# Optimization experiments

Measured on AMD Instinct MI355X. Metric: run time of the kernel, lower is better.

The kernel has to match this reference:

```python
import jax, jax.numpy as jnp
import numpy as np

B, D, H = 1024, 512, 128
S = D - 1
PI = float(np.pi)


def setup_inputs() -> dict:
    key = jax.random.key(0)
    k = jax.random.split(key, 4)
    # angles on the circle [0, 2*pi)
    z = jax.random.uniform(k[0], (B, D), dtype=jnp.float32) * (2.0 * PI)
    W1 = jax.random.normal(k[1], (S, D, H), dtype=jnp.float32) * 0.05
    b1 = jnp.zeros((S, H), dtype=jnp.float32)
    W2 = jax.random.normal(k[2], (S, H, 2), dtype=jnp.float32) * 0.05
    b2 = jnp.zeros((S, 2), dtype=jnp.float32)
    return {"z": z, "W1": W1, "b1": b1, "W2": W2, "b2": b2}


def reference(z, W1, b1, W2, b2):
    """IterativeARLayer.decode: sequential per-site conditioner + NCP diffeomorphism.

    Step idx conditions on z[:, :idx] (implemented as an input mask, identical math)
    and transforms site idx, accumulating log|det|.
    """
    Bn, Dn = z.shape
    Sn = Dn - 1
    # conditioner mask for step s transforms site idx=s+1, conditions on sites 0..s
    mask = (jnp.arange(Dn)[None, :] <= jnp.arange(Sn)[:, None]).astype(z.dtype)  # [S, D]
    idxs = jnp.arange(1, Dn)

    def step(carry, xs):
        x, log_det = carry
        w1, bb1, w2, bb2, m, idx = xs
        h = jax.nn.relu((z * m) @ w1 + bb1)          # [B, H]
        p = h @ w2 + bb2                              # [B, 2] unconstrained params
        alpha_raw, beta = p[:, 0], p[:, 1]
        a = jnp.exp(alpha_raw)
        # NCP diffeomorphism on site idx
        phi = z[:, idx]                               # [B]
        u = jnp.tan(0.5 * (phi - PI))
        v = a * u + beta
        out = 2.0 * jnp.arctan(v) + PI
        ld = alpha_raw + jnp.log1p(u * u) - jnp.log1p(v * v)
        x = x.at[:, idx].set(out)
        return (x, log_det + ld), None

    init = (z, jnp.zeros((Bn,), dtype=z.dtype))  # x = z.clone(); site 0 untouched
    (x, log_det), _ = jax.lax.scan(step, init, (W1, b1, W2, b2, mask, idxs))
    return x, log_det
```

## Files before the change

### kernel.cpp

```cpp
#include <hip/hip_runtime.h>
#include <math.h>

#define B_DIM 1024
#define D_DIM 512
#define H_DIM 128
#define S_DIM 511
#define PI_F 3.14159265358979323846f
#define ZSWZ_BYTES (8u * 1024u * 128u)
#define NTILES_TOTAL 2296
#define W1BF_BYTES ((size_t)NTILES_TOTAL * 16384)

typedef __attribute__((ext_vector_type(8))) short short8;
typedef __attribute__((ext_vector_type(4))) float f32x4;

static __device__ __forceinline__ unsigned cvt_pk_bf16(float lo, float hi) {
    unsigned r;
    asm("v_cvt_pk_bf16_f32 %0, %1, %2" : "=v"(r) : "v"(lo), "v"(hi));
    return r;
}

static __device__ __host__ __forceinline__ int tiles_before(int s) {
    const int q = s >> 6, r = s & 63;
    return s + 32 * q * (q - 1) + q * r;
}

__global__ __launch_bounds__(256) void pack_kernel(
        const float* __restrict__ z, const float* __restrict__ W1,
        unsigned char* __restrict__ z_swz, unsigned char* __restrict__ w1bf)
{
    if (blockIdx.x < 256) {
        const int gid = blockIdx.x * 256 + threadIdx.x;
        const int g   = gid & 7;
        const int row = (gid >> 3) & 1023;
        const int kt  = gid >> 13;
        const int srcg = g ^ (row & 7);
        const float* src = z + (size_t)row * D_DIM + kt * 64 + srcg * 8;
        float4 a = *(const float4*)src;
        float4 b = *(const float4*)(src + 4);
        uint4 w;
        w.x = cvt_pk_bf16(a.x, a.y);
        w.y = cvt_pk_bf16(a.z, a.w);
        w.z = cvt_pk_bf16(b.x, b.y);
        w.w = cvt_pk_bf16(b.z, b.w);
        *(uint4*)(z_swz + (size_t)kt * 131072 + row * 128 + g * 16) = w;
        return;
    }
    const int tb = blockIdx.x - 256;
    const int s  = tb >> 3;
    const int kk = tb & 7;
    if (s >= S_DIM || kk > (s >> 6)) return;
    const int k0 = kk << 6;
    const int t  = threadIdx.x;
    const int h2 = t & 63;
    const int mw = t >> 6;
    const float* __restrict__ W1s = W1 + (size_t)s * (D_DIM * H_DIM);
    unsigned char* out = w1bf + (size_t)(tiles_before(s) + kk) * 16384;
    const int h0 = h2 * 2, h1 = h2 * 2 + 1;
#pragma unroll
    for (int half = 0; half < 2; ++half) {
        const int m = mw + half * 4;
        float2 v[8];
#pragma unroll
        for (int e = 0; e < 8; ++e) {
            const int gk = k0 + m * 8 + e;
            v[e] = (gk <= s) ? *(const float2*)(W1s + (size_t)gk * H_DIM + h0)
                             : (float2){0.f, 0.f};
        }
        uint4 w0, w1;
        w0.x = cvt_pk_bf16(v[0].x, v[1].x); w0.y = cvt_pk_bf16(v[2].x, v[3].x);
        w0.z = cvt_pk_bf16(v[4].x, v[5].x); w0.w = cvt_pk_bf16(v[6].x, v[7].x);
        w1.x = cvt_pk_bf16(v[0].y, v[1].y); w1.y = cvt_pk_bf16(v[2].y, v[3].y);
        w1.z = cvt_pk_bf16(v[4].y, v[5].y); w1.w = cvt_pk_bf16(v[6].y, v[7].y);
        *(uint4*)(out + h0 * 128 + ((m ^ (h0 & 7)) << 4)) = w0;
        *(uint4*)(out + h1 * 128 + ((m ^ (h1 & 7)) << 4)) = w1;
    }
}

template<bool PRE>
__global__ __launch_bounds__(256) void ar_site_kernel(
        const float* __restrict__ z, const unsigned char* __restrict__ z_swz,
        const unsigned char* __restrict__ w1bf,
        const float* __restrict__ W1, const float* __restrict__ b1,
        const float* __restrict__ W2, const float* __restrict__ b2,
        float* __restrict__ x_out, float* __restrict__ ld_out)
{
    __shared__ __align__(16) unsigned char lds[73728];

    const int tid  = threadIdx.x;
    const int lane = tid & 63;
    const int wid  = tid >> 6;
    const int wr   = wid >> 1;
    const int wc   = wid & 1;
    const int l15  = lane & 15;
    const int l16  = lane >> 4;

    if (PRE) {
        const int ib   = blockIdx.x;
        const int c    = (((ib >> 3) & 7) << 3) | (ib & 7);
        const int bblk = ib >> 6;
        const int brow0 = bblk * 128;

        int pf_t = 0, pf_kk = 0, pf_step = 0;
        int pf_s = 510 - c;
        int pf_base = tiles_before(pf_s);

        auto pf_stage = [&]() {
            if (pf_t >= 8) return;
            const int slot = pf_step & 1;
            const unsigned char* srcA = z_swz + (size_t)pf_kk * 131072
                                        + (size_t)brow0 * 128 + wid * 4096 + lane * 16;
            const unsigned char* srcB = w1bf + (size_t)(pf_base + pf_kk) * 16384
                                        + wid * 4096 + lane * 16;
            unsigned char* dstA = lds + slot * 32768 + wid * 4096;
            unsigned char* dstB = lds + slot * 32768 + 16384 + wid * 4096;
#pragma unroll
            for (int i2 = 0; i2 < 4; ++i2) {
                __builtin_amdgcn_global_load_lds(
                    (const __attribute__((address_space(1))) unsigned int*)(srcA + i2 * 1024),
                    (__attribute__((address_space(3))) unsigned int*)(dstA + i2 * 1024),
                    16, 0, 0);
                __builtin_amdgcn_global_load_lds(
                    (const __attribute__((address_space(1))) unsigned int*)(srcB + i2 * 1024),
                    (__attribute__((address_space(3))) unsigned int*)(dstB + i2 * 1024),
                    16, 0, 0);
            }
            ++pf_step; ++pf_kk;
            if (pf_kk == ((pf_s >> 6) + 1)) {
                pf_kk = 0; ++pf_t;
                while (pf_t < 8) {
                    const int j = pf_t * 64 + ((pf_t & 1) ? (63 - c) : c);
                    if (j < S_DIM) { pf_s = 510 - j; pf_base = tiles_before(pf_s); break; }
                    ++pf_t;
                }
            }
        };

        int csteps = 0;
#pragma unroll
        for (int t = 0; t < 8; ++t) {
            const int j = t * 64 + ((t & 1) ? (63 - c) : c);
            if (j < S_DIM) csteps += ((510 - j) >> 6) + 1;
        }

        pf_stage();
        pf_stage();

        int step = 0;
        float ld_acc = 0.f;

        for (int t = 0; t < 8; ++t) {
            const int j = t * 64 + ((t & 1) ? (63 - c) : c);
            if (j >= S_DIM) continue;
            const int s   = 510 - j;
            const int nt  = (s >> 6) + 1;
            const int idx = s + 1;

            f32x4 acc[4][4];
#pragma unroll
            for (int mi = 0; mi < 4; ++mi)
#pragma unroll
                for (int ni = 0; ni < 4; ++ni)
                    acc[mi][ni] = (f32x4){0.f, 0.f, 0.f, 0.f};

            for (int kk = 0; kk < nt; ++kk) {
                if (step + 1 == csteps) {
                    asm volatile("s_waitcnt vmcnt(0)" ::: "memory");
                } else {
                    asm volatile("s_waitcnt vmcnt(8)" ::: "memory");
                }
                __builtin_amdgcn_s_barrier();
                __builtin_amdgcn_sched_barrier(0);
                const unsigned char* bufp = lds + (step & 1) * 32768;
#pragma unroll
                for (int ks = 0; ks < 2; ++ks) {
                    const int kb = ks * 64 + l16 * 16;
                    short8 af[4], bfr[4];
#pragma unroll
                    for (int mi = 0; mi < 4; ++mi) {
                        const int r = wr * 64 + mi * 16 + l15;
                        af[mi] = *(const short8*)(bufp + r * 128 + (kb ^ ((r & 7) << 4)));
                    }
#pragma unroll
                    for (int ni = 0; ni < 4; ++ni) {
                        const int h = wc * 64 + ni * 16 + l15;
                        bfr[ni] = *(const short8*)(bufp + 16384 + h * 128 + (kb ^ ((h & 7) << 4)));
                    }
                    __builtin_amdgcn_s_setprio(1);
#pragma unroll
                    for (int mi = 0; mi < 4; ++mi)
#pragma unroll
                        for (int ni = 0; ni < 4; ++ni)
                            acc[mi][ni] = __builtin_amdgcn_mfma_f32_16x16x32_bf16(
                                af[mi], bfr[ni], acc[mi][ni], 0, 0, 0);
                    __builtin_amdgcn_s_setprio(0);
                }
                __builtin_amdgcn_s_barrier();
                pf_stage();
                ++step;
            }

            float b1v[4], w2a[4], w2b[4];
#pragma unroll
            for (int ni = 0; ni < 4; ++ni) {
                const int cc = wc * 64 + ni * 16 + l15;
                b1v[ni] = b1[(size_t)s * H_DIM + cc];
                const float2 w2v = *(const float2*)(W2 + ((size_t)s * H_DIM + cc) * 2);
                w2a[ni] = w2v.x;
                w2b[ni] = w2v.y;
            }
            float p0s[4][4], p1s[4][4];
#pragma unroll
            for (int mi = 0; mi < 4; ++mi)
#pragma unroll
                for (int r = 0; r < 4; ++r) {
                    float p0 = 0.f, p1 = 0.f;
#pragma unroll
                    for (int ni = 0; ni < 4; ++ni) {
                        float h = acc[mi][ni][r] + b1v[ni];
                        h = fmaxf(h, 0.f);
                        p0 = fmaf(h, w2a[ni], p0);
                        p1 = fmaf(h, w2b[ni], p1);
                    }
                    p0s[mi][r] = p0; p1s[mi][r] = p1;
                }
#pragma unroll
            for (int mi = 0; mi < 4; ++mi)
#pragma unroll
                for (int r = 0; r < 4; ++r) {
                    p0s[mi][r] += __shfl_xor(p0s[mi][r], 1);
                    p0s[mi][r] += __shfl_xor(p0s[mi][r], 2);
                    p1s[mi][r] += __shfl_xor(p1s[mi][r], 1);
                    p1s[mi][r] += __shfl_xor(p1s[mi][r], 2);
                }
            if ((lane & 3) == 0) {
                const int cw = wc * 4 + (l15 >> 2);
#pragma unroll
                for (int mi = 0; mi < 4; ++mi)
#pragma unroll
                    for (int r = 0; r < 4; ++r) {
                        const int row = wr * 64 + mi * 16 + l16 * 4 + r;
                        *(float2*)(lds + 65536 + (row * 8 + (cw ^ (row & 7))) * 8)
                            = (float2){p0s[mi][r], p1s[mi][r]};
                    }
            }
            asm volatile("s_waitcnt lgkmcnt(0)" ::: "memory");
            __builtin_amdgcn_s_barrier();
            __builtin_amdgcn_sched_barrier(0);
            if (tid < 128) {
                const int row = tid;
                float alpha = b2[(size_t)s * 2 + 0];
                float beta  = b2[(size_t)s * 2 + 1];
#pragma unroll
                for (int cw = 0; cw < 8; ++cw) {
                    const float2 v = *(const float2*)(lds + 65536 + (row * 8 + (cw ^ (row & 7))) * 8);
                    alpha += v.x; beta += v.y;
                }
                const int grow = brow0 + row;
                const float phi = z[(size_t)grow * D_DIM + idx];
                const float u = tanf(0.5f * (phi - PI_F));
                const float a = expf(alpha);
                const float v = fmaf(a, u, beta);
                x_out[(size_t)grow * D_DIM + idx] = 2.0f * atanf(v) + PI_F;
                ld_acc += alpha + log1pf(u * u) - log1pf(v * v);
            }
        }
        if (tid < 128) atomicAdd(ld_out + brow0 + tid, ld_acc);
        if (c == 0 && tid < 128)
            x_out[(size_t)(brow0 + tid) * D_DIM] = z[(size_t)(brow0 + tid) * D_DIM];
        return;
    }

    const int ib    = blockIdx.x;
    const int s_idx = ((ib >> 6) << 3) | (ib & 7);
    if (s_idx >= S_DIM) return;
    const int s     = S_DIM - 1 - s_idx;
    const int bblk  = (ib >> 3) & 7;
    const int brow0 = bblk * 128;
    const int K     = s + 1;
    const int idx   = s + 1;
    const float* __restrict__ W1s = W1 + (size_t)s * (D_DIM * H_DIM);

    f32x4 acc[4][4];
#pragma unroll
    for (int mi = 0; mi < 4; ++mi)
#pragma unroll
        for (int ni = 0; ni < 4; ++ni)
            acc[mi][ni] = (f32x4){0.f, 0.f, 0.f, 0.f};

    const int ntiles = (K + 63) >> 6;
    for (int kk = 0; kk < ntiles; ++kk) {
        const int k0 = kk << 6;
        const int g  = tid & 7;
        const int rb = tid >> 3;
#pragma unroll
        for (int p = 0; p < 4; ++p) {
            const int row  = p * 32 + rb;
            const int srcg = g ^ (row & 7);
            const float* zp = z + (size_t)(brow0 + row) * D_DIM + k0 + srcg * 8;
            float4 va = *(const float4*)zp;
            float4 vb = *(const float4*)(zp + 4);
            uint4 w;
            w.x = cvt_pk_bf16(va.x, va.y);
            w.y = cvt_pk_bf16(va.z, va.w);
            w.z = cvt_pk_bf16(vb.x, vb.y);
            w.w = cvt_pk_bf16(vb.z, vb.w);
            *(uint4*)(lds + row * 128 + g * 16) = w;
        }
        const int hgrp  = tid & 31;
        const int kgrp  = tid >> 5;
        const int kbase = k0 + kgrp * 8;
        const float* wp = W1s + (size_t)kbase * H_DIM + hgrp * 4;
        float4 cc[8];
#pragma unroll
        for (int jj = 0; jj < 8; ++jj) {
            float4 v = *(const float4*)(wp + (size_t)jj * H_DIM);
            const bool ok = (kbase + jj) < K;
            v.x = ok ? v.x : 0.f;  v.y = ok ? v.y : 0.f;
            v.z = ok ? v.z : 0.f;  v.w = ok ? v.w : 0.f;
            cc[jj] = v;
        }
        const float* cf = (const float*)cc;
#pragma unroll
        for (int i2 = 0; i2 < 4; ++i2) {
            const int h = hgrp * 4 + i2;
            uint4 w;
            w.x = cvt_pk_bf16(cf[0 * 4 + i2], cf[1 * 4 + i2]);
            w.y = cvt_pk_bf16(cf[2 * 4 + i2], cf[3 * 4 + i2]);
            w.z = cvt_pk_bf16(cf[4 * 4 + i2], cf[5 * 4 + i2]);
            w.w = cvt_pk_bf16(cf[6 * 4 + i2], cf[7 * 4 + i2]);
            *(uint4*)(lds + 16384 + h * 128 + ((kgrp * 16) ^ ((h & 7) << 4))) = w;
        }
        __syncthreads();
#pragma unroll
        for (int ks = 0; ks < 2; ++ks) {
            const int kb = ks * 64 + l16 * 16;
            short8 af[4], bfr[4];
#pragma unroll
            for (int mi = 0; mi < 4; ++mi) {
                const int r = wr * 64 + mi * 16 + l15;
                af[mi] = *(const short8*)(lds + r * 128 + (kb ^ ((r & 7) << 4)));
            }
#pragma unroll
            for (int ni = 0; ni < 4; ++ni) {
                const int h = wc * 64 + ni * 16 + l15;
                bfr[ni] = *(const short8*)(lds + 16384 + h * 128 + (kb ^ ((h & 7) << 4)));
            }
#pragma unroll
            for (int mi = 0; mi < 4; ++mi)
#pragma unroll
                for (int ni = 0; ni < 4; ++ni)
                    acc[mi][ni] = __builtin_amdgcn_mfma_f32_16x16x32_bf16(
                        af[mi], bfr[ni], acc[mi][ni], 0, 0, 0);
        }
        __syncthreads();
    }

    float b1v[4], w2a[4], w2b[4];
#pragma unroll
    for (int ni = 0; ni < 4; ++ni) {
        const int cc2 = wc * 64 + ni * 16 + l15;
        b1v[ni] = b1[(size_t)s * H_DIM + cc2];
        const float* w2p = W2 + ((size_t)s * H_DIM + cc2) * 2;
        w2a[ni] = w2p[0];
        w2b[ni] = w2p[1];
    }
    float p0s[4][4], p1s[4][4];
#pragma unroll
    for (int mi = 0; mi < 4; ++mi)
#pragma unroll
        for (int r = 0; r < 4; ++r) {
            float p0 = 0.f, p1 = 0.f;
#pragma unroll
            for (int ni = 0; ni < 4; ++ni) {
                float h = acc[mi][ni][r] + b1v[ni];
                h = fmaxf(h, 0.f);
                p0 = fmaf(h, w2a[ni], p0);
                p1 = fmaf(h, w2b[ni], p1);
            }
            p0s[mi][r] = p0; p1s[mi][r] = p1;
        }
#pragma unroll
    for (int mi = 0; mi < 4; ++mi)
#pragma unroll
        for (int r = 0; r < 4; ++r) {
            p0s[mi][r] += __shfl_xor(p0s[mi][r], 1);
            p0s[mi][r] += __shfl_xor(p0s[mi][r], 2);
            p1s[mi][r] += __shfl_xor(p1s[mi][r], 1);
            p1s[mi][r] += __shfl_xor(p1s[mi][r], 2);
        }
    if ((lane & 3) == 0) {
        const int cw = wc * 4 + (l15 >> 2);
#pragma unroll
        for (int mi = 0; mi < 4; ++mi)
#pragma unroll
            for (int r = 0; r < 4; ++r) {
                const int row = wr * 64 + mi * 16 + l16 * 4 + r;
                *(float2*)(lds + 65536 + (row * 8 + (cw ^ (row & 7))) * 8)
                    = (float2){p0s[mi][r], p1s[mi][r]};
            }
    }
    __syncthreads();
    if (tid < 128) {
        const int row = tid;
        float alpha = b2[(size_t)s * 2 + 0];
        float beta  = b2[(size_t)s * 2 + 1];
#pragma unroll
        for (int cw = 0; cw < 8; ++cw) {
            const float2 v = *(const float2*)(lds + 65536 + (row * 8 + (cw ^ (row & 7))) * 8);
            alpha += v.x; beta += v.y;
        }
        const int grow = brow0 + row;
        const float phi = z[(size_t)grow * D_DIM + idx];
        const float u = tanf(0.5f * (phi - PI_F));
        const float a = expf(alpha);
        const float v = fmaf(a, u, beta);
        x_out[(size_t)grow * D_DIM + idx] = 2.0f * atanf(v) + PI_F;
        atomicAdd(ld_out + grow, alpha + log1pf(u * u) - log1pf(v * v));
        if (s_idx == 0)
            x_out[(size_t)grow * D_DIM] = z[(size_t)grow * D_DIM];
    }
}

extern "C" void kernel_launch(void* const* d_in, const int* in_sizes, int n_in,
                              void* d_out, int out_size, void* d_ws, size_t ws_size,
                              hipStream_t stream) {
    const float* z  = (const float*)d_in[0];
    const float* W1 = (const float*)d_in[1];
    const float* b1 = (const float*)d_in[2];
    const float* W2 = (const float*)d_in[3];
    const float* b2 = (const float*)d_in[4];
    float* x_out  = (float*)d_out;
    float* ld_out = x_out + (size_t)B_DIM * D_DIM;

    unsigned char* z_swz = (unsigned char*)d_ws;
    unsigned char* w1bf  = z_swz + ZSWZ_BYTES;
    const size_t need = ZSWZ_BYTES + W1BF_BYTES;

    hipMemsetAsync(ld_out, 0, B_DIM * sizeof(float), stream);
    if (ws_size >= need) {
        pack_kernel<<<dim3(256 + 4088), dim3(256), 0, stream>>>(z, W1, z_swz, w1bf);
        ar_site_kernel<true><<<dim3(512), dim3(256), 0, stream>>>(
            z, z_swz, w1bf, W1, b1, W2, b2, x_out, ld_out);
    } else {
        ar_site_kernel<false><<<dim3(4096), dim3(256), 0, stream>>>(
            z, nullptr, nullptr, W1, b1, W2, b2, x_out, ld_out);
    }
}
```

Before: 107.3 us.

## Use 32-wide K tiles, 8-wave blocks and 4-stage LDS prefetch pipeline

Repacks z and W1 into 32-wide K tiles with a new swizzle and tile indexing, and moves the precomputed path to 512-thread blocks. Each wave now computes a 64x32 slice, and the prefetch is split so half the waves load A and half load B. The double buffer becomes a 4-slot ring with three tiles in flight, one barrier per K step and graded vmcnt waits. The aim is to hide global-load latency and raise wave-level parallelism per CU. The cost is more K iterations, finer-grained loads, a wider shuffle reduction in the epilogue and more register pressure per block.

```diff
diff --git a/kernel.cpp b/kernel.cpp
--- a/kernel.cpp
+++ b/kernel.cpp
@@ -6,12 +6,18 @@
 #define H_DIM 128
 #define S_DIM 511
 #define PI_F 3.14159265358979323846f
-#define ZSWZ_BYTES (8u * 1024u * 128u)
-#define NTILES_TOTAL 2296
-#define W1BF_BYTES ((size_t)NTILES_TOTAL * 16384)
+#define ZSWZ_BYTES (16u * 1024u * 64u)
+#define NT32_TOTAL 4336
+#define W1BF_BYTES ((size_t)NT32_TOTAL * 8192)
+#define EPI_OFF 65536
 
 typedef __attribute__((ext_vector_type(8))) short short8;
 typedef __attribute__((ext_vector_type(4))) float f32x4;
+
+#define GLDS16(src, dst)                                                        \
+    __builtin_amdgcn_global_load_lds(                                           \
+        (const __attribute__((address_space(1))) unsigned int*)(src),           \
+        (__attribute__((address_space(3))) unsigned int*)(dst), 16, 0, 0)
 
 static __device__ __forceinline__ unsigned cvt_pk_bf16(float lo, float hi) {
     unsigned r;
@@ -19,9 +25,9 @@
     return r;
 }
 
-static __device__ __host__ __forceinline__ int tiles_before(int s) {
-    const int q = s >> 6, r = s & 63;
-    return s + 32 * q * (q - 1) + q * r;
+static __device__ __forceinline__ int tb32(int s) {
+    const int q = s >> 5, r = s & 31;
+    return 16 * q * (q + 1) + r * (q + 1);
 }
 
 __global__ __launch_bounds__(256) void pack_kernel(
@@ -30,11 +36,11 @@
 {
     if (blockIdx.x < 256) {
         const int gid = blockIdx.x * 256 + threadIdx.x;
-        const int g   = gid & 7;
-        const int row = (gid >> 3) & 1023;
-        const int kt  = gid >> 13;
-        const int srcg = g ^ (row & 7);
-        const float* src = z + (size_t)row * D_DIM + kt * 64 + srcg * 8;
+        const int g   = gid & 3;
+        const int row = (gid >> 2) & 1023;
+        const int kt  = gid >> 12;
+        const int srcg = g ^ ((row >> 1) & 3);
+        const float* src = z + (size_t)row * D_DIM + kt * 32 + srcg * 8;
         float4 a = *(const float4*)src;
         float4 b = *(const float4*)(src + 4);
         uint4 w;
@@ -42,42 +48,39 @@
         w.y = cvt_pk_bf16(a.z, a.w);
         w.z = cvt_pk_bf16(b.x, b.y);
         w.w = cvt_pk_bf16(b.z, b.w);
-        *(uint4*)(z_swz + (size_t)kt * 131072 + row * 128 + g * 16) = w;
+        *(uint4*)(z_swz + (size_t)kt * 65536 + row * 64 + g * 16) = w;
         return;
     }
     const int tb = blockIdx.x - 256;
-    const int s  = tb >> 3;
-    const int kk = tb & 7;
-    if (s >= S_DIM || kk > (s >> 6)) return;
-    const int k0 = kk << 6;
+    const int s  = tb >> 4;
+    const int kk = tb & 15;
+    if (s >= S_DIM || kk > (s >> 5)) return;
+    const int k0 = kk << 5;
     const int t  = threadIdx.x;
     const int h2 = t & 63;
     const int mw = t >> 6;
     const float* __restrict__ W1s = W1 + (size_t)s * (D_DIM * H_DIM);
-    unsigned char* out = w1bf + (size_t)(tiles_before(s) + kk) * 16384;
+    unsigned char* out = w1bf + (size_t)(tb32(s) + kk) * 8192;
     const int h0 = h2 * 2, h1 = h2 * 2 + 1;
-#pragma unroll
-    for (int half = 0; half < 2; ++half) {
-        const int m = mw + half * 4;
-        float2 v[8];
-#pragma unroll
-        for (int e = 0; e < 8; ++e) {
-            const int gk = k0 + m * 8 + e;
-            v[e] = (gk <= s) ? *(const float2*)(W1s + (size_t)gk * H_DIM + h0)
-                             : (float2){0.f, 0.f};
-        }
-        uint4 w0, w1;
-        w0.x = cvt_pk_bf16(v[0].x, v[1].x); w0.y = cvt_pk_bf16(v[2].x, v[3].x);
-        w0.z = cvt_pk_bf16(v[4].x, v[5].x); w0.w = cvt_pk_bf16(v[6].x, v[7].x);
-        w1.x = cvt_pk_bf16(v[0].y, v[1].y); w1.y = cvt_pk_bf16(v[2].y, v[3].y);
-        w1.z = cvt_pk_bf16(v[4].y, v[5].y); w1.w = cvt_pk_bf16(v[6].y, v[7].y);
-        *(uint4*)(out + h0 * 128 + ((m ^ (h0 & 7)) << 4)) = w0;
-        *(uint4*)(out + h1 * 128 + ((m ^ (h1 & 7)) << 4)) = w1;
-    }
+    const int slot = mw ^ (h2 & 3);
+    float2 v[8];
+#pragma unroll
+    for (int e = 0; e < 8; ++e) {
+        const int gk = k0 + mw * 8 + e;
+        v[e] = (gk <= s) ? *(const float2*)(W1s + (size_t)gk * H_DIM + h0)
+                         : (float2){0.f, 0.f};
+    }
+    uint4 w0, w1;
+    w0.x = cvt_pk_bf16(v[0].x, v[1].x); w0.y = cvt_pk_bf16(v[2].x, v[3].x);
+    w0.z = cvt_pk_bf16(v[4].x, v[5].x); w0.w = cvt_pk_bf16(v[6].x, v[7].x);
+    w1.x = cvt_pk_bf16(v[0].y, v[1].y); w1.y = cvt_pk_bf16(v[2].y, v[3].y);
+    w1.z = cvt_pk_bf16(v[4].y, v[5].y); w1.w = cvt_pk_bf16(v[6].y, v[7].y);
+    *(uint4*)(out + h0 * 64 + slot * 16) = w0;
+    *(uint4*)(out + h1 * 64 + slot * 16) = w1;
 }
 
 template<bool PRE>
-__global__ __launch_bounds__(256) void ar_site_kernel(
+__global__ __launch_bounds__(512, 4) void ar_site_kernel(
         const float* __restrict__ z, const unsigned char* __restrict__ z_swz,
         const unsigned char* __restrict__ w1bf,
         const float* __restrict__ W1, const float* __restrict__ b1,
@@ -89,12 +92,12 @@
     const int tid  = threadIdx.x;
     const int lane = tid & 63;
     const int wid  = tid >> 6;
-    const int wr   = wid >> 1;
-    const int wc   = wid & 1;
     const int l15  = lane & 15;
     const int l16  = lane >> 4;
 
     if (PRE) {
+        const int wr   = wid >> 2;
+        const int wc   = wid & 3;
         const int ib   = blockIdx.x;
         const int c    = (((ib >> 3) & 7) << 3) | (ib & 7);
         const int bblk = ib >> 6;
@@ -102,34 +105,31 @@
 
         int pf_t = 0, pf_kk = 0, pf_step = 0;
         int pf_s = 510 - c;
-        int pf_base = tiles_before(pf_s);
+        int pf_base = tb32(pf_s);
 
         auto pf_stage = [&]() {
             if (pf_t >= 8) return;
-            const int slot = pf_step & 1;
-            const unsigned char* srcA = z_swz + (size_t)pf_kk * 131072
-                                        + (size_t)brow0 * 128 + wid * 4096 + lane * 16;
-            const unsigned char* srcB = w1bf + (size_t)(pf_base + pf_kk) * 16384
-                                        + wid * 4096 + lane * 16;
-            unsigned char* dstA = lds + slot * 32768 + wid * 4096;
-            unsigned char* dstB = lds + slot * 32768 + 16384 + wid * 4096;
-#pragma unroll
-            for (int i2 = 0; i2 < 4; ++i2) {
-                __builtin_amdgcn_global_load_lds(
-                    (const __attribute__((address_space(1))) unsigned int*)(srcA + i2 * 1024),
-                    (__attribute__((address_space(3))) unsigned int*)(dstA + i2 * 1024),
-                    16, 0, 0);
-                __builtin_amdgcn_global_load_lds(
-                    (const __attribute__((address_space(1))) unsigned int*)(srcB + i2 * 1024),
-                    (__attribute__((address_space(3))) unsigned int*)(dstB + i2 * 1024),
-                    16, 0, 0);
+            unsigned char* slotp = lds + (pf_step & 3) * 16384;
+            if (wid < 4) {
+                const unsigned char* srcA = z_swz + (size_t)pf_kk * 65536
+                    + (size_t)(brow0 + wid * 32) * 64 + lane * 16;
+                unsigned char* dstA = slotp + wid * 2048;
+                GLDS16(srcA, dstA);
+                GLDS16(srcA + 1024, dstA + 1024);
+            } else {
+                const int w2 = wid - 4;
+                const unsigned char* srcB = w1bf + (size_t)(pf_base + pf_kk) * 8192
+                    + (size_t)(w2 * 32) * 64 + lane * 16;
+                unsigned char* dstB = slotp + 8192 + w2 * 2048;
+                GLDS16(srcB, dstB);
+                GLDS16(srcB + 1024, dstB + 1024);
             }
             ++pf_step; ++pf_kk;
-            if (pf_kk == ((pf_s >> 6) + 1)) {
+            if (pf_kk == (pf_s >> 5) + 1) {
                 pf_kk = 0; ++pf_t;
                 while (pf_t < 8) {
                     const int j = pf_t * 64 + ((pf_t & 1) ? (63 - c) : c);
-                    if (j < S_DIM) { pf_s = 510 - j; pf_base = tiles_before(pf_s); break; }
+                    if (j < S_DIM) { pf_s = 510 - j; pf_base = tb32(pf_s); break; }
                     ++pf_t;
                 }
             }
@@ -139,11 +139,10 @@
 #pragma unroll
         for (int t = 0; t < 8; ++t) {
             const int j = t * 64 + ((t & 1) ? (63 - c) : c);
-            if (j < S_DIM) csteps += ((510 - j) >> 6) + 1;
-        }
-
-        pf_stage();
-        pf_stage();
+            if (j < S_DIM) csteps += ((510 - j) >> 5) + 1;
+        }
+
+        pf_stage(); pf_stage(); pf_stage();
 
         int step = 0;
         float ld_acc = 0.f;
@@ -152,96 +151,83 @@
             const int j = t * 64 + ((t & 1) ? (63 - c) : c);
             if (j >= S_DIM) continue;
             const int s   = 510 - j;
-            const int nt  = (s >> 6) + 1;
+            const int nt  = (s >> 5) + 1;
             const int idx = s + 1;
 
-            f32x4 acc[4][4];
+            f32x4 acc[4][2];
 #pragma unroll
             for (int mi = 0; mi < 4; ++mi)
 #pragma unroll
-                for (int ni = 0; ni < 4; ++ni)
+                for (int ni = 0; ni < 2; ++ni)
                     acc[mi][ni] = (f32x4){0.f, 0.f, 0.f, 0.f};
 
             for (int kk = 0; kk < nt; ++kk) {
-                if (step + 1 == csteps) {
-                    asm volatile("s_waitcnt vmcnt(0)" ::: "memory");
-                } else {
-                    asm volatile("s_waitcnt vmcnt(8)" ::: "memory");
-                }
+                if (step + 2 < csteps)      asm volatile("s_waitcnt vmcnt(4)" ::: "memory");
+                else if (step + 1 < csteps) asm volatile("s_waitcnt vmcnt(2)" ::: "memory");
+                else                        asm volatile("s_waitcnt vmcnt(0)" ::: "memory");
                 __builtin_amdgcn_s_barrier();
                 __builtin_amdgcn_sched_barrier(0);
-                const unsigned char* bufp = lds + (step & 1) * 32768;
-#pragma unroll
-                for (int ks = 0; ks < 2; ++ks) {
-                    const int kb = ks * 64 + l16 * 16;
-                    short8 af[4], bfr[4];
-#pragma unroll
-                    for (int mi = 0; mi < 4; ++mi) {
-                        const int r = wr * 64 + mi * 16 + l15;
-                        af[mi] = *(const short8*)(bufp + r * 128 + (kb ^ ((r & 7) << 4)));
-                    }
-#pragma unroll
-                    for (int ni = 0; ni < 4; ++ni) {
-                        const int h = wc * 64 + ni * 16 + l15;
-                        bfr[ni] = *(const short8*)(bufp + 16384 + h * 128 + (kb ^ ((h & 7) << 4)));
-                    }
-                    __builtin_amdgcn_s_setprio(1);
-#pragma unroll
-                    for (int mi = 0; mi < 4; ++mi)
-#pragma unroll
-                        for (int ni = 0; ni < 4; ++ni)
-                            acc[mi][ni] = __builtin_amdgcn_mfma_f32_16x16x32_bf16(
-                                af[mi], bfr[ni], acc[mi][ni], 0, 0, 0);
-                    __builtin_amdgcn_s_setprio(0);
-                }
-                __builtin_amdgcn_s_barrier();
                 pf_stage();
+                const unsigned char* bufp = lds + (step & 3) * 16384;
+                short8 af[4], bfr[2];
+#pragma unroll
+                for (int ni = 0; ni < 2; ++ni) {
+                    const int h = wc * 32 + ni * 16 + l15;
+                    bfr[ni] = *(const short8*)(bufp + 8192 + h * 64
+                                               + ((l16 * 16) ^ ((((h >> 1) & 3)) << 4)));
+                }
+#pragma unroll
+                for (int mi = 0; mi < 4; ++mi) {
+                    const int r = wr * 64 + mi * 16 + l15;
+                    af[mi] = *(const short8*)(bufp + r * 64
+                                              + ((l16 * 16) ^ ((((r >> 1) & 3)) << 4)));
+                }
+                __builtin_amdgcn_s_setprio(1);
+#pragma unroll
+                for (int mi = 0; mi < 4; ++mi)
+#pragma unroll
+                    for (int ni = 0; ni < 2; ++ni)
+                        acc[mi][ni] = __builtin_amdgcn_mfma_f32_16x16x32_bf16(
+                            af[mi], bfr[ni], acc[mi][ni], 0, 0, 0);
+                __builtin_amdgcn_s_setprio(0);
                 ++step;
             }
 
-            float b1v[4], w2a[4], w2b[4];
-#pragma unroll
-            for (int ni = 0; ni < 4; ++ni) {
-                const int cc = wc * 64 + ni * 16 + l15;
+            float b1v[2], w2a[2], w2b[2];
+#pragma unroll
+            for (int ni = 0; ni < 2; ++ni) {
+                const int cc = wc * 32 + ni * 16 + l15;
                 b1v[ni] = b1[(size_t)s * H_DIM + cc];
                 const float2 w2v = *(const float2*)(W2 + ((size_t)s * H_DIM + cc) * 2);
                 w2a[ni] = w2v.x;
                 w2b[ni] = w2v.y;
             }
-            float p0s[4][4], p1s[4][4];
-#pragma unroll
-            for (int mi = 0; mi < 4; ++mi)
+#pragma unroll
+            for (int mi = 0; mi < 4; ++mi) {
+                float p0[4], p1[4];
 #pragma unroll
                 for (int r = 0; r < 4; ++r) {
-                    float p0 = 0.f, p1 = 0.f;
-#pragma unroll
-                    for (int ni = 0; ni < 4; ++ni) {
-                        float h = acc[mi][ni][r] + b1v[ni];
-                        h = fmaxf(h, 0.f);
-                        p0 = fmaf(h, w2a[ni], p0);
-                        p1 = fmaf(h, w2b[ni], p1);
+                    float a0 = 0.f, a1 = 0.f;
+#pragma unroll
+                    for (int ni = 0; ni < 2; ++ni) {
+                        float h = fmaxf(acc[mi][ni][r] + b1v[ni], 0.f);
+                        a0 = fmaf(h, w2a[ni], a0);
+                        a1 = fmaf(h, w2b[ni], a1);
                     }
-                    p0s[mi][r] = p0; p1s[mi][r] = p1;
-                }
-#pragma unroll
-            for (int mi = 0; mi < 4; ++mi)
-#pragma unroll
-                for (int r = 0; r < 4; ++r) {
-                    p0s[mi][r] += __shfl_xor(p0s[mi][r], 1);
-                    p0s[mi][r] += __shfl_xor(p0s[mi][r], 2);
-                    p1s[mi][r] += __shfl_xor(p1s[mi][r], 1);
-                    p1s[mi][r] += __shfl_xor(p1s[mi][r], 2);
-                }
-            if ((lane & 3) == 0) {
-                const int cw = wc * 4 + (l15 >> 2);
-#pragma unroll
-                for (int mi = 0; mi < 4; ++mi)
-#pragma unroll
-                    for (int r = 0; r < 4; ++r) {
-                        const int row = wr * 64 + mi * 16 + l16 * 4 + r;
-                        *(float2*)(lds + 65536 + (row * 8 + (cw ^ (row & 7))) * 8)
-                            = (float2){p0s[mi][r], p1s[mi][r]};
-                    }
+                    a0 += __shfl_xor(a0, 1); a0 += __shfl_xor(a0, 2);
+                    a0 += __shfl_xor(a0, 4); a0 += __shfl_xor(a0, 8);
+                    a1 += __shfl_xor(a1, 1); a1 += __shfl_xor(a1, 2);
+                    a1 += __shfl_xor(a1, 4); a1 += __shfl_xor(a1, 8);
+                    p0[r] = a0; p1[r] = a1;
+                }
+                if (l15 == 0) {
+                    const int rowb = wr * 64 + mi * 16 + l16 * 4;
+                    const int slot = (wc ^ (rowb >> 2)) & 3;
+#pragma unroll
+                    for (int r = 0; r < 4; ++r)
+                        *(float2*)(lds + EPI_OFF + (rowb + r) * 32 + slot * 8)
+                            = (float2){p0[r], p1[r]};
+                }
             }
             asm volatile("s_waitcnt lgkmcnt(0)" ::: "memory");
             __builtin_amdgcn_s_barrier();
@@ -251,8 +237,8 @@
                 float alpha = b2[(size_t)s * 2 + 0];
                 float beta  = b2[(size_t)s * 2 + 1];
 #pragma unroll
-                for (int cw = 0; cw < 8; ++cw) {
-                    const float2 v = *(const float2*)(lds + 65536 + (row * 8 + (cw ^ (row & 7))) * 8);
+                for (int p = 0; p < 4; ++p) {
+                    const float2 v = *(const float2*)(lds + EPI_OFF + row * 32 + p * 8);
                     alpha += v.x; beta += v.y;
                 }
                 const int grow = brow0 + row;
@@ -270,6 +256,7 @@
         return;
     }
 
+    const int wr2 = wid >> 1, wc2 = wid & 1;
     const int ib    = blockIdx.x;
     const int s_idx = ((ib >> 6) << 3) | (ib & 7);
     if (s_idx >= S_DIM) return;
@@ -337,12 +324,12 @@
             short8 af[4], bfr[4];
 #pragma unroll
             for (int mi = 0; mi < 4; ++mi) {
-                const int r = wr * 64 + mi * 16 + l15;
+                const int r = wr2 * 64 + mi * 16 + l15;
                 af[mi] = *(const short8*)(lds + r * 128 + (kb ^ ((r & 7) << 4)));
             }
 #pragma unroll
             for (int ni = 0; ni < 4; ++ni) {
-                const int h = wc * 64 + ni * 16 + l15;
+                const int h = wc2 * 64 + ni * 16 + l15;
                 bfr[ni] = *(const short8*)(lds + 16384 + h * 128 + (kb ^ ((h & 7) << 4)));
             }
 #pragma unroll
@@ -358,7 +345,7 @@
     float b1v[4], w2a[4], w2b[4];
 #pragma unroll
     for (int ni = 0; ni < 4; ++ni) {
-        const int cc2 = wc * 64 + ni * 16 + l15;
+        const int cc2 = wc2 * 64 + ni * 16 + l15;
         b1v[ni] = b1[(size_t)s * H_DIM + cc2];
         const float* w2p = W2 + ((size_t)s * H_DIM + cc2) * 2;
         w2a[ni] = w2p[0];
@@ -389,13 +376,13 @@
             p1s[mi][r] += __shfl_xor(p1s[mi][r], 2);
         }
     if ((lane & 3) == 0) {
-        const int cw = wc * 4 + (l15 >> 2);
+        const int cw = wc2 * 4 + (l15 >> 2);
 #pragma unroll
         for (int mi = 0; mi < 4; ++mi)
 #pragma unroll
             for (int r = 0; r < 4; ++r) {
-                const int row = wr * 64 + mi * 16 + l16 * 4 + r;
-                *(float2*)(lds + 65536 + (row * 8 + (cw ^ (row & 7))) * 8)
+                const int row = wr2 * 64 + mi * 16 + l16 * 4 + r;
+                *(float2*)(lds + EPI_OFF + (row * 8 + (cw ^ (row & 7))) * 8)
                     = (float2){p0s[mi][r], p1s[mi][r]};
             }
     }
@@ -406,7 +393,7 @@
         float beta  = b2[(size_t)s * 2 + 1];
 #pragma unroll
         for (int cw = 0; cw < 8; ++cw) {
-            const float2 v = *(const float2*)(lds + 65536 + (row * 8 + (cw ^ (row & 7))) * 8);
+            const float2 v = *(const float2*)(lds + EPI_OFF + (row * 8 + (cw ^ (row & 7))) * 8);
             alpha += v.x; beta += v.y;
         }
         const int grow = brow0 + row;
@@ -438,8 +425,8 @@
 
     hipMemsetAsync(ld_out, 0, B_DIM * sizeof(float), stream);
     if (ws_size >= need) {
-        pack_kernel<<<dim3(256 + 4088), dim3(256), 0, stream>>>(z, W1, z_swz, w1bf);
-        ar_site_kernel<true><<<dim3(512), dim3(256), 0, stream>>>(
+        pack_kernel<<<dim3(256 + 511 * 16), dim3(256), 0, stream>>>(z, W1, z_swz, w1bf);
+        ar_site_kernel<true><<<dim3(512), dim3(512), 0, stream>>>(
             z, z_swz, w1bf, W1, b1, W2, b2, x_out, ld_out);
     } else {
         ar_site_kernel<false><<<dim3(4096), dim3(256), 0, stream>>>(
```

Measured after the change: 138.8 us. 29.3% more time.

## Restructure double-buffered prefetch to one barrier per k-step and request two blocks/CU

Applied to the files above, without the earlier changes.

The main loop now waits for all outstanding loads, takes a single barrier, and only then issues the next tile's global-to-LDS prefetch into the other buffer before running the two MFMA k-halves. This replaces the old two-deep prefetch with vmcnt(8) throttling and a trailing barrier. The aim is to cut per-step synchronization. The cost is a shallower prefetch, so each load has only one tile's compute to hide behind. Launch bounds also request two blocks per CU to raise occupancy, which may force fewer registers per thread.

```diff
diff --git a/kernel.cpp b/kernel.cpp
--- a/kernel.cpp
+++ b/kernel.cpp
@@ -9,9 +9,15 @@
 #define ZSWZ_BYTES (8u * 1024u * 128u)
 #define NTILES_TOTAL 2296
 #define W1BF_BYTES ((size_t)NTILES_TOTAL * 16384)
+#define EPI_OFF 65536
 
 typedef __attribute__((ext_vector_type(8))) short short8;
 typedef __attribute__((ext_vector_type(4))) float f32x4;
+
+#define GLDS16(src, dst)                                                        \
+    __builtin_amdgcn_global_load_lds(                                           \
+        (const __attribute__((address_space(1))) unsigned int*)(src),           \
+        (__attribute__((address_space(3))) unsigned int*)(dst), 16, 0, 0)
 
 static __device__ __forceinline__ unsigned cvt_pk_bf16(float lo, float hi) {
     unsigned r;
@@ -19,7 +25,7 @@
     return r;
 }
 
-static __device__ __host__ __forceinline__ int tiles_before(int s) {
+static __device__ __forceinline__ int tiles_before(int s) {
     const int q = s >> 6, r = s & 63;
     return s + 32 * q * (q - 1) + q * r;
 }
@@ -77,7 +83,7 @@
 }
 
 template<bool PRE>
-__global__ __launch_bounds__(256) void ar_site_kernel(
+__global__ __launch_bounds__(256, 2) void ar_site_kernel(
         const float* __restrict__ z, const unsigned char* __restrict__ z_swz,
         const unsigned char* __restrict__ w1bf,
         const float* __restrict__ W1, const float* __restrict__ b1,
@@ -115,14 +121,8 @@
             unsigned char* dstB = lds + slot * 32768 + 16384 + wid * 4096;
 #pragma unroll
             for (int i2 = 0; i2 < 4; ++i2) {
-                __builtin_amdgcn_global_load_lds(
-                    (const __attribute__((address_space(1))) unsigned int*)(srcA + i2 * 1024),
-                    (__attribute__((address_space(3))) unsigned int*)(dstA + i2 * 1024),
-                    16, 0, 0);
-                __builtin_amdgcn_global_load_lds(
-                    (const __attribute__((address_space(1))) unsigned int*)(srcB + i2 * 1024),
-                    (__attribute__((address_space(3))) unsigned int*)(dstB + i2 * 1024),
-                    16, 0, 0);
+                GLDS16(srcA + i2 * 1024, dstA + i2 * 1024);
+                GLDS16(srcB + i2 * 1024, dstB + i2 * 1024);
             }
             ++pf_step; ++pf_kk;
             if (pf_kk == ((pf_s >> 6) + 1)) {
@@ -135,14 +135,6 @@
             }
         };
 
-        int csteps = 0;
-#pragma unroll
-        for (int t = 0; t < 8; ++t) {
-            const int j = t * 64 + ((t & 1) ? (63 - c) : c);
-            if (j < S_DIM) csteps += ((510 - j) >> 6) + 1;
-        }
-
-        pf_stage();
         pf_stage();
 
         int step = 0;
@@ -163,39 +155,57 @@
                     acc[mi][ni] = (f32x4){0.f, 0.f, 0.f, 0.f};
 
             for (int kk = 0; kk < nt; ++kk) {
-                if (step + 1 == csteps) {
-                    asm volatile("s_waitcnt vmcnt(0)" ::: "memory");
-                } else {
-                    asm volatile("s_waitcnt vmcnt(8)" ::: "memory");
-                }
+                asm volatile("s_waitcnt vmcnt(0)" ::: "memory");
                 __builtin_amdgcn_s_barrier();
                 __builtin_amdgcn_sched_barrier(0);
                 const unsigned char* bufp = lds + (step & 1) * 32768;
-#pragma unroll
-                for (int ks = 0; ks < 2; ++ks) {
-                    const int kb = ks * 64 + l16 * 16;
-                    short8 af[4], bfr[4];
+
+                pf_stage();
+
+                short8 af0[4], bf0[4], af1[4], bf1[4];
+                {
+                    const int kb = l16 * 16;
 #pragma unroll
                     for (int mi = 0; mi < 4; ++mi) {
                         const int r = wr * 64 + mi * 16 + l15;
-                        af[mi] = *(const short8*)(bufp + r * 128 + (kb ^ ((r & 7) << 4)));
+                        af0[mi] = *(const short8*)(bufp + r * 128 + (kb ^ ((r & 7) << 4)));
                     }
 #pragma unroll
                     for (int ni = 0; ni < 4; ++ni) {
                         const int h = wc * 64 + ni * 16 + l15;
-                        bfr[ni] = *(const short8*)(bufp + 16384 + h * 128 + (kb ^ ((h & 7) << 4)));
-                    }
-                    __builtin_amdgcn_s_setprio(1);
-#pragma unroll
-                    for (int mi = 0; mi < 4; ++mi)
-#pragma unroll
-                        for (int ni = 0; ni < 4; ++ni)
-                            acc[mi][ni] = __builtin_amdgcn_mfma_f32_16x16x32_bf16(
-                                af[mi], bfr[ni], acc[mi][ni], 0, 0, 0);
-                    __builtin_amdgcn_s_setprio(0);
-                }
-                __builtin_amdgcn_s_barrier();
-                pf_stage();
+                        bf0[ni] = *(const short8*)(bufp + 16384 + h * 128 + (kb ^ ((h & 7) << 4)));
+                    }
+                }
+                __builtin_amdgcn_s_setprio(1);
+#pragma unroll
+                for (int mi = 0; mi < 4; ++mi)
+#pragma unroll
+                    for (int ni = 0; ni < 4; ++ni)
+                        acc[mi][ni] = __builtin_amdgcn_mfma_f32_16x16x32_bf16(
+                            af0[mi], bf0[ni], acc[mi][ni], 0, 0, 0);
+                __builtin_amdgcn_s_setprio(0);
+
+                {
+                    const int kb = 64 + l16 * 16;
+#pragma unroll
+                    for (int mi = 0; mi < 4; ++mi) {
+                        const int r = wr * 64 + mi * 16 + l15;
+                        af1[mi] = *(const short8*)(bufp + r * 128 + (kb ^ ((r & 7) << 4)));
+                    }
+#pragma unroll
+                    for (int ni = 0; ni < 4; ++ni) {
+                        const int h = wc * 64 + ni * 16 + l15;
+                        bf1[ni] = *(const short8*)(bufp + 16384 + h * 128 + (kb ^ ((h & 7) << 4)));
+                    }
+                }
+                __builtin_amdgcn_s_setprio(1);
+#pragma unroll
+                for (int mi = 0; mi < 4; ++mi)
+#pragma unroll
+                    for (int ni = 0; ni < 4; ++ni)
+                        acc[mi][ni] = __builtin_amdgcn_mfma_f32_16x16x32_bf16(
+                            af1[mi], bf1[ni], acc[mi][ni], 0, 0, 0);
+                __builtin_amdgcn_s_setprio(0);
                 ++step;
             }
 
@@ -239,7 +249,7 @@
 #pragma unroll
                     for (int r = 0; r < 4; ++r) {
                         const int row = wr * 64 + mi * 16 + l16 * 4 + r;
-                        *(float2*)(lds + 65536 + (row * 8 + (cw ^ (row & 7))) * 8)
+                        *(float2*)(lds + EPI_OFF + (row * 8 + (cw ^ (row & 7))) * 8)
                             = (float2){p0s[mi][r], p1s[mi][r]};
                     }
             }
@@ -252,7 +262,7 @@
                 float beta  = b2[(size_t)s * 2 + 1];
 #pragma unroll
                 for (int cw = 0; cw < 8; ++cw) {
-                    const float2 v = *(const float2*)(lds + 65536 + (row * 8 + (cw ^ (row & 7))) * 8);
+                    const float2 v = *(const float2*)(lds + EPI_OFF + (row * 8 + (cw ^ (row & 7))) * 8);
                     alpha += v.x; beta += v.y;
                 }
                 const int grow = brow0 + row;
@@ -395,7 +405,7 @@
 #pragma unroll
             for (int r = 0; r < 4; ++r) {
                 const int row = wr * 64 + mi * 16 + l16 * 4 + r;
-                *(float2*)(lds + 65536 + (row * 8 + (cw ^ (row & 7))) * 8)
+                *(float2*)(lds + EPI_OFF + (row * 8 + (cw ^ (row & 7))) * 8)
                     = (float2){p0s[mi][r], p1s[mi][r]};
             }
     }
@@ -406,7 +416,7 @@
         float beta  = b2[(size_t)s * 2 + 1];
 #pragma unroll
         for (int cw = 0; cw < 8; ++cw) {
-            const float2 v = *(const float2*)(lds + 65536 + (row * 8 + (cw ^ (row & 7))) * 8);
+            const float2 v = *(const float2*)(lds + EPI_OFF + (row * 8 + (cw ^ (row & 7))) * 8);
             alpha += v.x; beta += v.y;
         }
         const int grow = brow0 + row;
```

After: 107.1 us. About the same (-0.3%).

## Pack operands in MFMA fragment order and load directly to registers

Applied to the files above, without the earlier changes.

The pack kernel now writes z and W1 bf16 tiles in MFMA fragment order, so each lane can load its A/B fragments from global memory into registers. This replaces the LDS double-buffer staging (global_load_lds plus barriers) with a register double buffer. The goal is to remove LDS traffic and block-wide barriers in the K loop. In exchange, register pressure rises (4 sets of 8 short8), each wave reloads shared tiles separately so global/L2 traffic goes up, and an extra __syncthreads is added per site for the epilogue LDS reuse.

```diff
diff --git a/kernel.cpp b/kernel.cpp
--- a/kernel.cpp
+++ b/kernel.cpp
@@ -19,22 +19,22 @@
     return r;
 }
 
-static __device__ __host__ __forceinline__ int tiles_before(int s) {
+static __device__ __forceinline__ int tiles_before(int s) {
     const int q = s >> 6, r = s & 63;
     return s + 32 * q * (q - 1) + q * r;
 }
 
+
 __global__ __launch_bounds__(256) void pack_kernel(
         const float* __restrict__ z, const float* __restrict__ W1,
-        unsigned char* __restrict__ z_swz, unsigned char* __restrict__ w1bf)
+        unsigned char* __restrict__ z_frag, unsigned char* __restrict__ w1bf)
 {
     if (blockIdx.x < 256) {
         const int gid = blockIdx.x * 256 + threadIdx.x;
         const int g   = gid & 7;
         const int row = (gid >> 3) & 1023;
         const int kt  = gid >> 13;
-        const int srcg = g ^ (row & 7);
-        const float* src = z + (size_t)row * D_DIM + kt * 64 + srcg * 8;
+        const float* src = z + (size_t)row * D_DIM + kt * 64 + g * 8;
         float4 a = *(const float4*)src;
         float4 b = *(const float4*)(src + 4);
         uint4 w;
@@ -42,7 +42,10 @@
         w.y = cvt_pk_bf16(a.z, a.w);
         w.z = cvt_pk_bf16(b.x, b.y);
         w.w = cvt_pk_bf16(b.z, b.w);
-        *(uint4*)(z_swz + (size_t)kt * 131072 + row * 128 + g * 16) = w;
+        const int r7 = row & 127;
+        const int tile = (row >> 7) * 8 + kt;
+        const int off = (((r7 >> 4) * 2 + (g >> 2)) << 10) + ((g & 3) << 8) + ((r7 & 15) << 4);
+        *(uint4*)(z_frag + (size_t)tile * 16384 + off) = w;
         return;
     }
     const int tb = blockIdx.x - 256;
@@ -71,20 +74,21 @@
         w0.z = cvt_pk_bf16(v[4].x, v[5].x); w0.w = cvt_pk_bf16(v[6].x, v[7].x);
         w1.x = cvt_pk_bf16(v[0].y, v[1].y); w1.y = cvt_pk_bf16(v[2].y, v[3].y);
         w1.z = cvt_pk_bf16(v[4].y, v[5].y); w1.w = cvt_pk_bf16(v[6].y, v[7].y);
-        *(uint4*)(out + h0 * 128 + ((m ^ (h0 & 7)) << 4)) = w0;
-        *(uint4*)(out + h1 * 128 + ((m ^ (h1 & 7)) << 4)) = w1;
+        const int base0 = (((h0 >> 4) * 2 + (m >> 2)) << 10) + ((m & 3) << 8);
+        *(uint4*)(out + base0 + ((h0 & 15) << 4)) = w0;
+        *(uint4*)(out + base0 + ((h1 & 15) << 4)) = w1;
     }
 }
 
 template<bool PRE>
 __global__ __launch_bounds__(256) void ar_site_kernel(
-        const float* __restrict__ z, const unsigned char* __restrict__ z_swz,
+        const float* __restrict__ z, const unsigned char* __restrict__ z_frag,
         const unsigned char* __restrict__ w1bf,
         const float* __restrict__ W1, const float* __restrict__ b1,
         const float* __restrict__ W2, const float* __restrict__ b2,
         float* __restrict__ x_out, float* __restrict__ ld_out)
 {
-    __shared__ __align__(16) unsigned char lds[73728];
+    __shared__ __align__(16) unsigned char lds[36864];
 
     const int tid  = threadIdx.x;
     const int lane = tid & 63;
@@ -95,57 +99,54 @@
     const int l16  = lane >> 4;
 
     if (PRE) {
+        const int epi = 0;
         const int ib   = blockIdx.x;
         const int c    = (((ib >> 3) & 7) << 3) | (ib & 7);
         const int bblk = ib >> 6;
         const int brow0 = bblk * 128;
 
-        int pf_t = 0, pf_kk = 0, pf_step = 0;
+        int pf_t = 0, pf_kk = 0;
         int pf_s = 510 - c;
         int pf_base = tiles_before(pf_s);
 
-        auto pf_stage = [&]() {
-            if (pf_t >= 8) return;
-            const int slot = pf_step & 1;
-            const unsigned char* srcA = z_swz + (size_t)pf_kk * 131072
-                                        + (size_t)brow0 * 128 + wid * 4096 + lane * 16;
-            const unsigned char* srcB = w1bf + (size_t)(pf_base + pf_kk) * 16384
-                                        + wid * 4096 + lane * 16;
-            unsigned char* dstA = lds + slot * 32768 + wid * 4096;
-            unsigned char* dstB = lds + slot * 32768 + 16384 + wid * 4096;
-#pragma unroll
-            for (int i2 = 0; i2 < 4; ++i2) {
-                __builtin_amdgcn_global_load_lds(
-                    (const __attribute__((address_space(1))) unsigned int*)(srcA + i2 * 1024),
-                    (__attribute__((address_space(3))) unsigned int*)(dstA + i2 * 1024),
-                    16, 0, 0);
-                __builtin_amdgcn_global_load_lds(
-                    (const __attribute__((address_space(1))) unsigned int*)(srcB + i2 * 1024),
-                    (__attribute__((address_space(3))) unsigned int*)(dstB + i2 * 1024),
-                    16, 0, 0);
-            }
-            ++pf_step; ++pf_kk;
-            if (pf_kk == ((pf_s >> 6) + 1)) {
-                pf_kk = 0; ++pf_t;
-                while (pf_t < 8) {
-                    const int j = pf_t * 64 + ((pf_t & 1) ? (63 - c) : c);
-                    if (j < S_DIM) { pf_s = 510 - j; pf_base = tiles_before(pf_s); break; }
-                    ++pf_t;
-                }
-            }
-        };
-
-        int csteps = 0;
-#pragma unroll
-        for (int t = 0; t < 8; ++t) {
-            const int j = t * 64 + ((t & 1) ? (63 - c) : c);
-            if (j < S_DIM) csteps += ((510 - j) >> 6) + 1;
-        }
-
-        pf_stage();
-        pf_stage();
-
-        int step = 0;
+        short8 A0[8], B0[8], A1[8], B1[8];
+
+#define STEP_LOAD(NA, NB)                                                       \
+        if (pf_t < 8) {                                                         \
+            const unsigned char* ab = z_frag + (((size_t)(bblk * 8 + pf_kk)) << 14) \
+                                      + (wr * 8 << 10) + lane * 16;             \
+            const unsigned char* bb = w1bf + (((size_t)(pf_base + pf_kk)) << 14)    \
+                                      + (wc * 8 << 10) + lane * 16;             \
+            _Pragma("unroll")                                                   \
+            for (int i = 0; i < 8; ++i) {                                       \
+                NA[i] = *(const short8*)(ab + i * 1024);                        \
+                NB[i] = *(const short8*)(bb + i * 1024);                        \
+            }                                                                   \
+            ++pf_kk;                                                            \
+            if (pf_kk == ((pf_s >> 6) + 1)) {                                   \
+                pf_kk = 0; ++pf_t;                                              \
+                while (pf_t < 8) {                                              \
+                    const int jj = pf_t * 64 + ((pf_t & 1) ? (63 - c) : c);     \
+                    if (jj < S_DIM) { pf_s = 510 - jj; pf_base = tiles_before(pf_s); break; } \
+                    ++pf_t;                                                     \
+                }                                                               \
+            }                                                                   \
+        }
+
+#define STEP_MFMA(CA, CB)                                                       \
+        __builtin_amdgcn_s_setprio(1);                                          \
+        _Pragma("unroll")                                                       \
+        for (int ks = 0; ks < 2; ++ks)                                          \
+            _Pragma("unroll")                                                   \
+            for (int mi = 0; mi < 4; ++mi)                                      \
+                _Pragma("unroll")                                               \
+                for (int ni = 0; ni < 4; ++ni)                                  \
+                    acc[mi][ni] = __builtin_amdgcn_mfma_f32_16x16x32_bf16(      \
+                        CA[mi * 2 + ks], CB[ni * 2 + ks], acc[mi][ni], 0, 0, 0);\
+        __builtin_amdgcn_s_setprio(0);
+
+        STEP_LOAD(A0, B0);
+        int parity = 0;
         float ld_acc = 0.f;
 
         for (int t = 0; t < 8; ++t) {
@@ -163,40 +164,15 @@
                     acc[mi][ni] = (f32x4){0.f, 0.f, 0.f, 0.f};
 
             for (int kk = 0; kk < nt; ++kk) {
-                if (step + 1 == csteps) {
-                    asm volatile("s_waitcnt vmcnt(0)" ::: "memory");
+                if (parity == 0) {
+                    STEP_LOAD(A1, B1);
+                    STEP_MFMA(A0, B0);
+                    parity = 1;
                 } else {
-                    asm volatile("s_waitcnt vmcnt(8)" ::: "memory");
+                    STEP_LOAD(A0, B0);
+                    STEP_MFMA(A1, B1);
+                    parity = 0;
                 }
-                __builtin_amdgcn_s_barrier();
-                __builtin_amdgcn_sched_barrier(0);
-                const unsigned char* bufp = lds + (step & 1) * 32768;
-#pragma unroll
-                for (int ks = 0; ks < 2; ++ks) {
-                    const int kb = ks * 64 + l16 * 16;
-                    short8 af[4], bfr[4];
-#pragma unroll
-                    for (int mi = 0; mi < 4; ++mi) {
-                        const int r = wr * 64 + mi * 16 + l15;
-                        af[mi] = *(const short8*)(bufp + r * 128 + (kb ^ ((r & 7) << 4)));
-                    }
-#pragma unroll
-                    for (int ni = 0; ni < 4; ++ni) {
-                        const int h = wc * 64 + ni * 16 + l15;
-                        bfr[ni] = *(const short8*)(bufp + 16384 + h * 128 + (kb ^ ((h & 7) << 4)));
-                    }
-                    __builtin_amdgcn_s_setprio(1);
-#pragma unroll
-                    for (int mi = 0; mi < 4; ++mi)
-#pragma unroll
-                        for (int ni = 0; ni < 4; ++ni)
-                            acc[mi][ni] = __builtin_amdgcn_mfma_f32_16x16x32_bf16(
-                                af[mi], bfr[ni], acc[mi][ni], 0, 0, 0);
-                    __builtin_amdgcn_s_setprio(0);
-                }
-                __builtin_amdgcn_s_barrier();
-                pf_stage();
-                ++step;
             }
 
             float b1v[4], w2a[4], w2b[4];
@@ -216,8 +192,7 @@
                     float p0 = 0.f, p1 = 0.f;
 #pragma unroll
                     for (int ni = 0; ni < 4; ++ni) {
-                        float h = acc[mi][ni][r] + b1v[ni];
-                        h = fmaxf(h, 0.f);
+                        float h = fmaxf(acc[mi][ni][r] + b1v[ni], 0.f);
                         p0 = fmaf(h, w2a[ni], p0);
                         p1 = fmaf(h, w2b[ni], p1);
                     }
@@ -239,20 +214,18 @@
 #pragma unroll
                     for (int r = 0; r < 4; ++r) {
                         const int row = wr * 64 + mi * 16 + l16 * 4 + r;
-                        *(float2*)(lds + 65536 + (row * 8 + (cw ^ (row & 7))) * 8)
+                        *(float2*)(lds + epi + (row * 8 + (cw ^ (row & 7))) * 8)
                             = (float2){p0s[mi][r], p1s[mi][r]};
                     }
             }
-            asm volatile("s_waitcnt lgkmcnt(0)" ::: "memory");
-            __builtin_amdgcn_s_barrier();
-            __builtin_amdgcn_sched_barrier(0);
+            __syncthreads();
             if (tid < 128) {
                 const int row = tid;
                 float alpha = b2[(size_t)s * 2 + 0];
                 float beta  = b2[(size_t)s * 2 + 1];
 #pragma unroll
                 for (int cw = 0; cw < 8; ++cw) {
-                    const float2 v = *(const float2*)(lds + 65536 + (row * 8 + (cw ^ (row & 7))) * 8);
+                    const float2 v = *(const float2*)(lds + epi + (row * 8 + (cw ^ (row & 7))) * 8);
                     alpha += v.x; beta += v.y;
                 }
                 const int grow = brow0 + row;
@@ -263,13 +236,17 @@
                 x_out[(size_t)grow * D_DIM + idx] = 2.0f * atanf(v) + PI_F;
                 ld_acc += alpha + log1pf(u * u) - log1pf(v * v);
             }
+            __syncthreads();
         }
         if (tid < 128) atomicAdd(ld_out + brow0 + tid, ld_acc);
         if (c == 0 && tid < 128)
             x_out[(size_t)(brow0 + tid) * D_DIM] = z[(size_t)(brow0 + tid) * D_DIM];
         return;
-    }
-
+#undef STEP_LOAD
+#undef STEP_MFMA
+    }
+
+    const int EPI2 = 32768;
     const int ib    = blockIdx.x;
     const int s_idx = ((ib >> 6) << 3) | (ib & 7);
     if (s_idx >= S_DIM) return;
@@ -372,8 +349,7 @@
             float p0 = 0.f, p1 = 0.f;
 #pragma unroll
             for (int ni = 0; ni < 4; ++ni) {
-                float h = acc[mi][ni][r] + b1v[ni];
-                h = fmaxf(h, 0.f);
+                float h = fmaxf(acc[mi][ni][r] + b1v[ni], 0.f);
                 p0 = fmaf(h, w2a[ni], p0);
                 p1 = fmaf(h, w2b[ni], p1);
             }
@@ -395,7 +371,7 @@
 #pragma unroll
             for (int r = 0; r < 4; ++r) {
                 const int row = wr * 64 + mi * 16 + l16 * 4 + r;
-                *(float2*)(lds + 65536 + (row * 8 + (cw ^ (row & 7))) * 8)
+                *(float2*)(lds + EPI2 + (row * 8 + (cw ^ (row & 7))) * 8)
                     = (float2){p0s[mi][r], p1s[mi][r]};
             }
     }
@@ -406,7 +382,7 @@
         float beta  = b2[(size_t)s * 2 + 1];
 #pragma unroll
         for (int cw = 0; cw < 8; ++cw) {
-            const float2 v = *(const float2*)(lds + 65536 + (row * 8 + (cw ^ (row & 7))) * 8);
+            const float2 v = *(const float2*)(lds + EPI2 + (row * 8 + (cw ^ (row & 7))) * 8);
             alpha += v.x; beta += v.y;
         }
         const int grow = brow0 + row;
@@ -432,15 +408,15 @@
     float* x_out  = (float*)d_out;
     float* ld_out = x_out + (size_t)B_DIM * D_DIM;
 
-    unsigned char* z_swz = (unsigned char*)d_ws;
-    unsigned char* w1bf  = z_swz + ZSWZ_BYTES;
+    unsigned char* z_frag = (unsigned char*)d_ws;
+    unsigned char* w1bf   = z_frag + ZSWZ_BYTES;
     const size_t need = ZSWZ_BYTES + W1BF_BYTES;
 
     hipMemsetAsync(ld_out, 0, B_DIM * sizeof(float), stream);
     if (ws_size >= need) {
-        pack_kernel<<<dim3(256 + 4088), dim3(256), 0, stream>>>(z, W1, z_swz, w1bf);
+        pack_kernel<<<dim3(256 + 4088), dim3(256), 0, stream>>>(z, W1, z_frag, w1bf);
         ar_site_kernel<true><<<dim3(512), dim3(256), 0, stream>>>(
-            z, z_swz, w1bf, W1, b1, W2, b2, x_out, ld_out);
+            z, z_frag, w1bf, W1, b1, W2, b2, x_out, ld_out);
     } else {
         ar_site_kernel<false><<<dim3(4096), dim3(256), 0, stream>>>(
             z, nullptr, nullptr, W1, b1, W2, b2, x_out, ld_out);
```

After: 132.7 us. +23.6%, slower.
